# Performance work log

Hardware: AMD Instinct MI355X
Metric: run time of the kernel (lower is better)

## Reference

```python
import jax, jax.numpy as jnp
import numpy as np

D_MODEL = 1024

def setup_inputs() -> dict:
    key = jax.random.key(0)
    ks = jax.random.split(key, 5)
    s = 1.0 / np.sqrt(D_MODEL)  # torch Linear default init scale-ish
    x = jax.random.normal(ks[0], (4, 2048, D_MODEL), dtype=jnp.float32)
    Wq = jax.random.normal(ks[1], (D_MODEL, D_MODEL), dtype=jnp.float32) * s
    Wk = jax.random.normal(ks[2], (D_MODEL, D_MODEL), dtype=jnp.float32) * s
    Wv = jax.random.normal(ks[3], (D_MODEL, D_MODEL), dtype=jnp.float32) * s
    Wo = jax.random.normal(ks[4], (D_MODEL, D_MODEL), dtype=jnp.float32) * s
    z = jnp.zeros((D_MODEL,), dtype=jnp.float32)
    return {"x": x, "Wq": Wq, "bq": z, "Wk": Wk, "bk": z, "Wv": Wv, "bv": z, "Wo": Wo, "bo": z}

def reference(x, Wq, bq, Wk, bk, Wv, bv, Wo, bo):
    # x: (B, S, D). Single-head causal attention, dropout in eval mode (identity).
    B, S, D = x.shape
    Q = jnp.einsum('bsd,ed->bse', x, Wq) + bq
    K = jnp.einsum('bsd,ed->bse', x, Wk) + bk
    V = jnp.einsum('bsd,ed->bse', x, Wv) + bv
    scores = jnp.einsum('bqd,bkd->bqk', Q, K) / jnp.sqrt(jnp.float32(D))
    causal = jnp.tril(jnp.ones((S, S), dtype=bool))  # (S, S)
    scores = jnp.where(causal, scores, -jnp.inf)
    weights = jax.nn.softmax(scores, axis=-1)
    attended = jnp.einsum('bqk,bkd->bqd', weights, V)
    out = jnp.einsum('bsd,ed->bse', attended, Wo) + bo
    return out
```

## Files before the change

kernel.cpp:

```cpp
#include <hip/hip_runtime.h>
#include <cstdint>
#include <cstddef>


#define D_MODEL 1024
#define SEQ     2048
#define BATCH   4

typedef unsigned short u16;
typedef __bf16 bf16_t;
typedef bf16_t bf16x8 __attribute__((ext_vector_type(8)));
typedef float  f32x4  __attribute__((ext_vector_type(4)));
typedef u16    u16x4  __attribute__((ext_vector_type(4)));

__device__ __forceinline__ u16 f2bf(float x) {
  union { float f; uint32_t u; } v; v.f = x;
  uint32_t r = v.u + 0x7fffu + ((v.u >> 16) & 1u);
  return (u16)(r >> 16);
}
__device__ __forceinline__ float bf2f(u16 h) {
  union { uint32_t u; float f; } v; v.u = (uint32_t)h << 16;
  return v.f;
}

__device__ __forceinline__ void gload_lds16(const u16* g, u16* l) {
  __builtin_amdgcn_global_load_lds((__attribute__((address_space(1))) void*)g,
                                   (__attribute__((address_space(3))) void*)l,
                                   16, 0, 0);
}

__device__ __forceinline__ void gemm256(const u16* __restrict__ A,
                                        const u16* __restrict__ B,
                                        int lda, int ldb, int nt,
                                        u16* As, u16* Bs,
                                        f32x4 acc[8][4]) {
  const int tid  = threadIdx.x;
  const int lane = tid & 63, wave = tid >> 6;
  const int frow = lane & 15, kc = lane >> 4;
  const int abase = (wave >> 2) * 128, bbase = (wave & 3) * 64;
  const int r0 = tid >> 2;
  const int k0 = ((tid & 3) ^ ((r0 >> 1) & 3)) * 8;
  const u16* Asrc0 = A + (size_t)r0 * lda + k0;
  const u16* Asrc1 = A + (size_t)(r0 + 128) * lda + k0;
  const u16* Bsrc0 = B + (size_t)r0 * ldb + k0;
  const u16* Bsrc1 = B + (size_t)(r0 + 128) * ldb + k0;
  int aoff[8], boff[4];
#pragma unroll
  for (int i = 0; i < 8; ++i) {
    const int ra = abase + i * 16 + frow;
    aoff[i] = (ra * 4 + (kc ^ ((ra >> 1) & 3))) * 8;
  }
#pragma unroll
  for (int j = 0; j < 4; ++j) {
    const int rb = bbase + j * 16 + frow;
    boff[j] = (rb * 4 + (kc ^ ((rb >> 1) & 3))) * 8;
  }
  auto stage = [&](int t, int bufi) {
    u16* ab = As + bufi * 8192;
    u16* bb = Bs + bufi * 8192;
    const int kb = t * 32;
    gload_lds16(Asrc0 + kb, ab + tid * 8);
    gload_lds16(Asrc1 + kb, ab + 4096 + tid * 8);
    gload_lds16(Bsrc0 + kb, bb + tid * 8);
    gload_lds16(Bsrc1 + kb, bb + 4096 + tid * 8);
  };
  stage(0, 0);
  if (nt > 1) stage(1, 1);
  int cb = 0, sb = 2;
  for (int t = 0; t < nt; ++t) {
    if (t + 1 < nt) asm volatile("s_waitcnt vmcnt(4)" ::: "memory");
    else            asm volatile("s_waitcnt vmcnt(0)" ::: "memory");
    __builtin_amdgcn_s_barrier();
    asm volatile("" ::: "memory");
    if (t + 2 < nt) stage(t + 2, sb);
    const u16* ab = As + cb * 8192;
    const u16* bb = Bs + cb * 8192;
    bf16x8 af[8], bf[4];
#pragma unroll
    for (int j = 0; j < 4; ++j) bf[j] = *(const bf16x8*)(bb + boff[j]);
#pragma unroll
    for (int i = 0; i < 8; ++i) af[i] = *(const bf16x8*)(ab + aoff[i]);
    __builtin_amdgcn_s_setprio(1);
#pragma unroll
    for (int i = 0; i < 8; ++i)
#pragma unroll
      for (int j = 0; j < 4; ++j)
        acc[i][j] = __builtin_amdgcn_mfma_f32_16x16x32_bf16(af[i], bf[j], acc[i][j], 0, 0, 0);
    __builtin_amdgcn_s_setprio(0);
    asm volatile("" ::: "memory");
    cb = (cb == 2) ? 0 : cb + 1;
    sb = (sb == 2) ? 0 : sb + 1;
  }
}

__device__ __forceinline__ void gemm128(const u16* __restrict__ A,
                                        const u16* __restrict__ B,
                                        int lda, int ldb, int nt,
                                        u16* As, u16* Bs,
                                        f32x4 acc[4][2]) {
  const int tid  = threadIdx.x;
  const int lane = tid & 63, wave = tid >> 6;
  const int frow = lane & 15, kc = lane >> 4;
  const int abase = (wave >> 2) * 64, bbase = (wave & 3) * 32;
  const int r0 = tid >> 2;
  const int k0 = ((tid & 3) ^ ((r0 >> 1) & 3)) * 8;
  const u16* Asrc = A + (size_t)r0 * lda + k0;
  const u16* Bsrc = B + (size_t)r0 * ldb + k0;
  int aoff[4], boff[2];
#pragma unroll
  for (int i = 0; i < 4; ++i) {
    const int ra = abase + i * 16 + frow;
    aoff[i] = (ra * 4 + (kc ^ ((ra >> 1) & 3))) * 8;
  }
#pragma unroll
  for (int j = 0; j < 2; ++j) {
    const int rb = bbase + j * 16 + frow;
    boff[j] = (rb * 4 + (kc ^ ((rb >> 1) & 3))) * 8;
  }
  auto stage = [&](int t) {
    u16* ab = As + (t & 3) * 4096;
    u16* bb = Bs + (t & 3) * 4096;
    const int kb = t * 32;
    gload_lds16(Asrc + kb, ab + tid * 8);
    gload_lds16(Bsrc + kb, bb + tid * 8);
  };
  stage(0);
  if (nt > 1) stage(1);
  if (nt > 2) stage(2);
  for (int t = 0; t < nt; ++t) {
    if (t + 2 < nt)      asm volatile("s_waitcnt vmcnt(4)" ::: "memory");
    else if (t + 1 < nt) asm volatile("s_waitcnt vmcnt(2)" ::: "memory");
    else                 asm volatile("s_waitcnt vmcnt(0)" ::: "memory");
    __builtin_amdgcn_s_barrier();
    asm volatile("" ::: "memory");
    if (t + 3 < nt) stage(t + 3);
    const u16* ab = As + (t & 3) * 4096;
    const u16* bb = Bs + (t & 3) * 4096;
    bf16x8 af[4], bf[2];
#pragma unroll
    for (int j = 0; j < 2; ++j) bf[j] = *(const bf16x8*)(bb + boff[j]);
#pragma unroll
    for (int i = 0; i < 4; ++i) af[i] = *(const bf16x8*)(ab + aoff[i]);
    __builtin_amdgcn_s_setprio(1);
#pragma unroll
    for (int i = 0; i < 4; ++i)
#pragma unroll
      for (int j = 0; j < 2; ++j)
        acc[i][j] = __builtin_amdgcn_mfma_f32_16x16x32_bf16(af[i], bf[j], acc[i][j], 0, 0, 0);
    __builtin_amdgcn_s_setprio(0);
    asm volatile("" ::: "memory");
  }
}

__global__ __launch_bounds__(256) void cvt_kernel(const float4* __restrict__ x,
                                                  const float4* __restrict__ wq,
                                                  const float4* __restrict__ wk,
                                                  const float4* __restrict__ wv,
                                                  const float4* __restrict__ wo,
                                                  u16* __restrict__ dst) {
  const int i = blockIdx.x * 256 + threadIdx.x;
  float4 v;
  if (i < 2097152) {
    v = x[i];
  } else {
    const int j = i - 2097152;
    const int w = j >> 18;
    const float4* s = (w == 0) ? wq : (w == 1) ? wk : (w == 2) ? wv : wo;
    v = s[j & 262143];
  }
  u16x4 o = {f2bf(v.x), f2bf(v.y), f2bf(v.z), f2bf(v.w)};
  *(u16x4*)(dst + (size_t)i * 4) = o;
}

__global__ void transposeW_kernel(const u16* __restrict__ src, u16* __restrict__ dst) {
  __shared__ u16 tile[32][33];
  const int r0 = blockIdx.x * 32, c0 = blockIdx.y * 32;
  const int tx = threadIdx.x, ty = threadIdx.y;
#pragma unroll
  for (int r = 0; r < 4; ++r)
    tile[ty + r * 8][tx] = src[(size_t)(r0 + ty + r * 8) * D_MODEL + c0 + tx];
  __syncthreads();
#pragma unroll
  for (int r = 0; r < 4; ++r)
    dst[(size_t)(c0 + ty + r * 8) * D_MODEL + r0 + tx] = tile[tx][ty + r * 8];
}

__global__ __launch_bounds__(512, 2) void stageA_kernel(
    const u16* __restrict__ xb,
    const u16* __restrict__ WqB, const u16* __restrict__ WkB,
    const u16* __restrict__ WoB, const u16* __restrict__ WvT,
    const float* __restrict__ Wo32, const float* __restrict__ bv,
    const float* __restrict__ bq, const float* __restrict__ bk,
    u16* __restrict__ Qb, u16* __restrict__ Kb,
    u16* __restrict__ Wp, float* __restrict__ bp) {
  __shared__ __align__(16) u16 As[24576];
  __shared__ __align__(16) u16 Bs[24576];
  const int blk = blockIdx.x, tid = threadIdx.x;
  const int lane = tid & 63, wave = tid >> 6;
  const int cl = lane & 15, rl = (lane >> 4) * 4;

  if (blk < 256) {
    const int c = blk & 7, i = blk >> 3;
    const int z = i >> 4, w = i & 15;
    const int rt = c * 4 + (w >> 2), ct = w & 3;
    const int row0 = rt * 256, col0 = ct * 256;
    const u16*   W    = z ? WkB : WqB;
    const float* bias = z ? bk : bq;
    u16*         out  = z ? Kb : Qb;
    f32x4 acc[8][4] = {};
    gemm256(xb + (size_t)row0 * D_MODEL, W + (size_t)col0 * D_MODEL,
            D_MODEL, D_MODEL, 32, As, Bs, acc);
    const int abase = (wave >> 2) * 128, bbase = (wave & 3) * 64;
#pragma unroll
    for (int j = 0; j < 4; ++j) {
      const int col = col0 + bbase + j * 16 + cl;
      const float bb = bias[col];
#pragma unroll
      for (int ii = 0; ii < 8; ++ii)
#pragma unroll
        for (int r = 0; r < 4; ++r) {
          const int row = row0 + abase + ii * 16 + rl + r;
          out[(size_t)row * D_MODEL + col] = f2bf(acc[ii][j][r] + bb);
        }
    }
  } else if (blk < 320) {
    const int qq = blk - 256;
    const int t16 = qq >> 2, quad = qq & 3;
    const int f0 = (t16 >> 2) * 256 + (quad >> 1) * 128;
    const int e0 = (t16 & 3) * 256 + (quad & 1) * 128;
    f32x4 acc[4][2] = {};
    gemm128(WoB + (size_t)f0 * D_MODEL, WvT + (size_t)e0 * D_MODEL,
            D_MODEL, D_MODEL, 32, As, Bs, acc);
    const int abase = (wave >> 2) * 64, bbase = (wave & 3) * 32;
#pragma unroll
    for (int j = 0; j < 2; ++j) {
      const int col = e0 + bbase + j * 16 + cl;
#pragma unroll
      for (int ii = 0; ii < 4; ++ii)
#pragma unroll
        for (int r = 0; r < 4; ++r) {
          const int row = f0 + abase + ii * 16 + rl + r;
          Wp[(size_t)row * D_MODEL + col] = f2bf(acc[ii][j][r]);
        }
    }
  } else {
    const int f  = (blk - 320) * 64 + (tid >> 3);
    const int dq = tid & 7;
    const float* row = Wo32 + (size_t)f * D_MODEL + dq * 128;
    const float* bvq = bv + dq * 128;
    float s = 0.f;
#pragma unroll 8
    for (int k = 0; k < 128; ++k) s += row[k] * bvq[k];
    s += __shfl_xor(s, 1);
    s += __shfl_xor(s, 2);
    s += __shfl_xor(s, 4);
    if (dq == 0) bp[f] = s;
  }
}

__global__ __launch_bounds__(512, 2) void stageB_kernel(
    const u16* __restrict__ xb, const u16* __restrict__ Wp,
    const float* __restrict__ bp,
    const u16* __restrict__ Qb, const u16* __restrict__ Kb,
    u16* __restrict__ Vt, u16* __restrict__ Eb, float* __restrict__ rssum) {
  __shared__ __align__(16) u16 As[24576];
  __shared__ __align__(16) u16 Bs[24576];
  const int blk = blockIdx.x, tid = threadIdx.x;
  const int lane = tid & 63, wave = tid >> 6;
  const int cl = lane & 15, rl = (lane >> 4) * 4;

  if (blk < 144) {
    const int c = blk & 7, u = blk >> 3;
    const int b = c >> 1, h = c & 1;
    int qi, ji;
    if (h == 0) {
      if (u < 1)       { qi = 0; ji = u; }
      else if (u < 5)  { qi = 3; ji = u - 1; }
      else if (u < 10) { qi = 4; ji = u - 5; }
      else             { qi = 7; ji = u - 10; }
    } else {
      if (u < 2)       { qi = 1; ji = u; }
      else if (u < 5)  { qi = 2; ji = u - 2; }
      else if (u < 11) { qi = 5; ji = u - 5; }
      else             { qi = 6; ji = u - 11; }
    }
    const u16* A  = Qb + (size_t)(b * SEQ + qi * 256) * D_MODEL;
    const u16* Bt = Kb + (size_t)(b * SEQ + ji * 256) * D_MODEL;
    f32x4 acc[8][4] = {};
    gemm256(A, Bt, D_MODEL, D_MODEL, 32, As, Bs, acc);
    u16* outp = Eb + (size_t)b * SEQ * SEQ;
    float* rs = rssum + b * SEQ;
    const int abase = (wave >> 2) * 128, bbase = (wave & 3) * 64;
#pragma unroll
    for (int ii = 0; ii < 8; ++ii)
#pragma unroll
      for (int r = 0; r < 4; ++r) {
        const int q = qi * 256 + abase + ii * 16 + rl + r;
        float ps = 0.f;
#pragma unroll
        for (int j = 0; j < 4; ++j) {
          const int jj = ji * 256 + bbase + j * 16 + cl;
          u16 h16 = 0;
          if (jj <= q) h16 = f2bf(__expf(acc[ii][j][r] * 0.03125f));
          outp[(size_t)q * SEQ + jj] = h16;
          ps += bf2f(h16);
        }
        ps += __shfl_xor(ps, 1);
        ps += __shfl_xor(ps, 2);
        ps += __shfl_xor(ps, 4);
        ps += __shfl_xor(ps, 8);
        if (cl == 0) atomicAdd(&rs[q], ps);
      }
  } else if (blk < 256) {
    const int v = blk - 144;
    const int rt = v >> 2, ct = v & 3;
    const int row0 = rt * 256, col0 = ct * 256;
    f32x4 acc[8][4] = {};
    gemm256(xb + (size_t)row0 * D_MODEL, Wp + (size_t)col0 * D_MODEL,
            D_MODEL, D_MODEL, 32, As, Bs, acc);
    const int b = row0 >> 11;
    u16* vt = Vt + (size_t)b * D_MODEL * SEQ;
    const int abase = (wave >> 2) * 128, bbase = (wave & 3) * 64;
#pragma unroll
    for (int j = 0; j < 4; ++j) {
      const int col = col0 + bbase + j * 16 + cl;
      const float bb = bp[col];
#pragma unroll
      for (int ii = 0; ii < 8; ++ii) {
        const int s0 = (row0 & 2047) + abase + ii * 16 + rl;
        u16x4 o = {f2bf(acc[ii][j][0] + bb), f2bf(acc[ii][j][1] + bb),
                   f2bf(acc[ii][j][2] + bb), f2bf(acc[ii][j][3] + bb)};
        *(u16x4*)(vt + (size_t)col * SEQ + s0) = o;
      }
    }
  } else {
    const int qq = blk - 256;
    const int t16 = qq >> 2, quad = qq & 3;
    const int rt = 28 + (t16 >> 2), ct = t16 & 3;
    const int row0 = rt * 256 + (quad >> 1) * 128;
    const int col0 = ct * 256 + (quad & 1) * 128;
    f32x4 acc[4][2] = {};
    gemm128(xb + (size_t)row0 * D_MODEL, Wp + (size_t)col0 * D_MODEL,
            D_MODEL, D_MODEL, 32, As, Bs, acc);
    const int b = row0 >> 11;
    u16* vt = Vt + (size_t)b * D_MODEL * SEQ;
    const int abase = (wave >> 2) * 64, bbase = (wave & 3) * 32;
#pragma unroll
    for (int j = 0; j < 2; ++j) {
      const int col = col0 + bbase + j * 16 + cl;
      const float bb = bp[col];
#pragma unroll
      for (int ii = 0; ii < 4; ++ii) {
        const int s0 = (row0 & 2047) + abase + ii * 16 + rl;
        u16x4 o = {f2bf(acc[ii][j][0] + bb), f2bf(acc[ii][j][1] + bb),
                   f2bf(acc[ii][j][2] + bb), f2bf(acc[ii][j][3] + bb)};
        *(u16x4*)(vt + (size_t)col * SEQ + s0) = o;
      }
    }
  }
}

__global__ __launch_bounds__(512, 4) void pv_kernel(const u16* __restrict__ Eb,
                                                    const u16* __restrict__ Vt,
                                                    const float* __restrict__ rssum,
                                                    const float* __restrict__ bo,
                                                    float* __restrict__ Out) {
  __shared__ __align__(16) u16 As[16384];
  __shared__ __align__(16) u16 Bs[16384];
  const int blk = blockIdx.x, tid = threadIdx.x;
  const int rr = blk >> 8, idx = blk & 255;
  const int b = idx >> 6, rest = idx & 63;
  const int dt8 = rest >> 3, m = rest & 7;
  const int qt = rr ? (15 - 2 * m) : (2 * m);
  const u16* A  = Eb + (size_t)b * SEQ * SEQ + (size_t)(qt * 128) * SEQ;
  const u16* Bt = Vt + (size_t)b * D_MODEL * SEQ + (size_t)(dt8 * 128) * SEQ;
  f32x4 acc[4][2] = {};
  gemm128(A, Bt, SEQ, SEQ, (qt + 1) * 4, As, Bs, acc);
  const int lane = tid & 63, wave = tid >> 6;
  const int abase = (wave >> 2) * 64, bbase = (wave & 3) * 32;
  const int cl = lane & 15, rl = (lane >> 4) * 4;
#pragma unroll
  for (int ii = 0; ii < 4; ++ii)
#pragma unroll
    for (int r = 0; r < 4; ++r) {
      const int row = qt * 128 + abase + ii * 16 + rl + r;
      const float invl = 1.0f / rssum[b * SEQ + row];
#pragma unroll
      for (int j = 0; j < 2; ++j) {
        const int col = dt8 * 128 + bbase + j * 16 + cl;
        Out[(size_t)(b * SEQ + row) * D_MODEL + col] = acc[ii][j][r] * invl + bo[col];
      }
    }
}

extern "C" void kernel_launch(void* const* d_in, const int* in_sizes, int n_in,
                              void* d_out, int out_size, void* d_ws, size_t ws_size,
                              hipStream_t stream) {
  const float* x  = (const float*)d_in[0];
  const float* Wq = (const float*)d_in[1];
  const float* bq = (const float*)d_in[2];
  const float* Wk = (const float*)d_in[3];
  const float* bk = (const float*)d_in[4];
  const float* Wv = (const float*)d_in[5];
  const float* bv = (const float*)d_in[6];
  const float* Wo = (const float*)d_in[7];
  const float* bo = (const float*)d_in[8];
  float* out = (float*)d_out;
  char* ws = (char*)d_ws;

  u16*   xb  = (u16*)(ws);
  u16*   Wb  = (u16*)(ws + (16u << 20));
  u16*   Qb  = (u16*)(ws + (24u << 20));
  u16*   Kb  = (u16*)(ws + (40u << 20));
  u16*   Vt  = (u16*)(ws + (56u << 20));
  u16*   Eb  = (u16*)(ws + (72u << 20));
  u16*   WvT = (u16*)(ws + (104u << 20));
  u16*   Wp  = (u16*)(ws + (106u << 20));
  float* bp  = (float*)(ws + (108u << 20));
  float* rssum = (float*)(ws + (20u << 20));

  cvt_kernel<<<12288, 256, 0, stream>>>((const float4*)x, (const float4*)Wq,
                                        (const float4*)Wk, (const float4*)Wv,
                                        (const float4*)Wo, xb);
  transposeW_kernel<<<dim3(32, 32), dim3(32, 8), 0, stream>>>(Wb + (2u << 20), WvT);
  stageA_kernel<<<336, 512, 0, stream>>>(xb, Wb, Wb + (1u << 20), Wb + (3u << 20),
                                         WvT, Wo, bv, bq, bk, Qb, Kb, Wp, bp);
  hipMemsetAsync(rssum, 0, BATCH * SEQ * sizeof(float), stream);
  stageB_kernel<<<320, 512, 0, stream>>>(xb, Wp, bp, Qb, Kb, Vt, Eb, rssum);
  pv_kernel<<<512, 512, 0, stream>>>(Eb, Vt, rssum, bo, out);
}
```

Before: 269.0 us.

## Use BK=64 double-buffered gemm256 and 256x256 tiles in PV kernel

The 256x256 GEMM core now loads K-slices of 64 into two LDS buffers instead of 32-wide slices into a triple buffer. This halves the number of barrier/wait iterations, and the MFMA work is split into interleaved half-steps so LDS reads overlap compute. The PV kernel moves from 128x128 tiles (512 blocks) to 256x256 tiles via gemm256 (128 blocks) for more operand reuse. The cost is larger LDS use, lower PV occupancy, and possible load imbalance, because only 128 causally uneven blocks are launched.

Result: slower. 290.6 us (+8.0%).

```diff
diff --git a/kernel.cpp b/kernel.cpp
--- a/kernel.cpp
+++ b/kernel.cpp
@@ -31,65 +31,94 @@
 
 __device__ __forceinline__ void gemm256(const u16* __restrict__ A,
                                         const u16* __restrict__ B,
-                                        int lda, int ldb, int nt,
+                                        int lda, int ldb, int nt64,
                                         u16* As, u16* Bs,
                                         f32x4 acc[8][4]) {
   const int tid  = threadIdx.x;
   const int lane = tid & 63, wave = tid >> 6;
   const int frow = lane & 15, kc = lane >> 4;
   const int abase = (wave >> 2) * 128, bbase = (wave & 3) * 64;
-  const int r0 = tid >> 2;
-  const int k0 = ((tid & 3) ^ ((r0 >> 1) & 3)) * 8;
-  const u16* Asrc0 = A + (size_t)r0 * lda + k0;
-  const u16* Asrc1 = A + (size_t)(r0 + 128) * lda + k0;
-  const u16* Bsrc0 = B + (size_t)r0 * ldb + k0;
-  const u16* Bsrc1 = B + (size_t)(r0 + 128) * ldb + k0;
+  const int r8 = tid >> 3, cch = tid & 7;
+  const int swz = ((r8 & 1) << 2) | ((r8 >> 1) & 3);
+  const int g8 = (cch ^ swz) * 8;
+  const u16* Arow = A + (size_t)r8 * lda + g8;
+  const u16* Brow = B + (size_t)r8 * ldb + g8;
+  const size_t lda64 = (size_t)64 * lda, ldb64 = (size_t)64 * ldb;
   int aoff[8], boff[4];
 #pragma unroll
   for (int i = 0; i < 8; ++i) {
     const int ra = abase + i * 16 + frow;
-    aoff[i] = (ra * 4 + (kc ^ ((ra >> 1) & 3))) * 8;
+    const int c0 = (kc ^ ((ra >> 1) & 3)) ^ ((ra & 1) << 2);
+    aoff[i] = ra * 64 + c0 * 8;
   }
 #pragma unroll
   for (int j = 0; j < 4; ++j) {
     const int rb = bbase + j * 16 + frow;
-    boff[j] = (rb * 4 + (kc ^ ((rb >> 1) & 3))) * 8;
-  }
-  auto stage = [&](int t, int bufi) {
-    u16* ab = As + bufi * 8192;
-    u16* bb = Bs + bufi * 8192;
-    const int kb = t * 32;
-    gload_lds16(Asrc0 + kb, ab + tid * 8);
-    gload_lds16(Asrc1 + kb, ab + 4096 + tid * 8);
-    gload_lds16(Bsrc0 + kb, bb + tid * 8);
-    gload_lds16(Bsrc1 + kb, bb + 4096 + tid * 8);
+    const int c0 = (kc ^ ((rb >> 1) & 3)) ^ ((rb & 1) << 2);
+    boff[j] = rb * 64 + c0 * 8;
+  }
+  auto stage = [&](int t) {
+    u16* ab = As + (t & 1) * 16384;
+    u16* bb = Bs + (t & 1) * 16384;
+    const int kb = t * 64;
+#pragma unroll
+    for (int L = 0; L < 4; ++L)
+      gload_lds16(Arow + kb + L * lda64, ab + (L * 512 + tid) * 8);
+#pragma unroll
+    for (int L = 0; L < 4; ++L)
+      gload_lds16(Brow + kb + L * ldb64, bb + (L * 512 + tid) * 8);
   };
-  stage(0, 0);
-  if (nt > 1) stage(1, 1);
-  int cb = 0, sb = 2;
-  for (int t = 0; t < nt; ++t) {
-    if (t + 1 < nt) asm volatile("s_waitcnt vmcnt(4)" ::: "memory");
-    else            asm volatile("s_waitcnt vmcnt(0)" ::: "memory");
+  stage(0);
+  for (int t = 0; t < nt64; ++t) {
     __builtin_amdgcn_s_barrier();
-    asm volatile("" ::: "memory");
-    if (t + 2 < nt) stage(t + 2, sb);
-    const u16* ab = As + cb * 8192;
-    const u16* bb = Bs + cb * 8192;
-    bf16x8 af[8], bf[4];
-#pragma unroll
-    for (int j = 0; j < 4; ++j) bf[j] = *(const bf16x8*)(bb + boff[j]);
-#pragma unroll
-    for (int i = 0; i < 8; ++i) af[i] = *(const bf16x8*)(ab + aoff[i]);
+    if (t + 1 < nt64) {
+      stage(t + 1);
+      asm volatile("s_waitcnt vmcnt(8)" ::: "memory");
+    } else {
+      asm volatile("s_waitcnt vmcnt(0)" ::: "memory");
+    }
+    __builtin_amdgcn_s_barrier();
+    const u16* ab = As + (t & 1) * 16384;
+    const u16* bb = Bs + (t & 1) * 16384;
+    bf16x8 a0[4], a1[4], b0[4], b1[4];
+#pragma unroll
+    for (int j = 0; j < 4; ++j) b0[j] = *(const bf16x8*)(bb + boff[j]);
+#pragma unroll
+    for (int i = 0; i < 4; ++i) a0[i] = *(const bf16x8*)(ab + aoff[i]);
+#pragma unroll
+    for (int i = 0; i < 4; ++i) a1[i] = *(const bf16x8*)(ab + aoff[4 + i]);
     __builtin_amdgcn_s_setprio(1);
 #pragma unroll
-    for (int i = 0; i < 8; ++i)
+    for (int i = 0; i < 4; ++i)
 #pragma unroll
       for (int j = 0; j < 4; ++j)
-        acc[i][j] = __builtin_amdgcn_mfma_f32_16x16x32_bf16(af[i], bf[j], acc[i][j], 0, 0, 0);
+        acc[i][j] = __builtin_amdgcn_mfma_f32_16x16x32_bf16(a0[i], b0[j], acc[i][j], 0, 0, 0);
     __builtin_amdgcn_s_setprio(0);
-    asm volatile("" ::: "memory");
-    cb = (cb == 2) ? 0 : cb + 1;
-    sb = (sb == 2) ? 0 : sb + 1;
+#pragma unroll
+    for (int j = 0; j < 4; ++j) b1[j] = *(const bf16x8*)(bb + (boff[j] ^ 32));
+#pragma unroll
+    for (int i = 0; i < 4; ++i) a0[i] = *(const bf16x8*)(ab + (aoff[i] ^ 32));
+    __builtin_amdgcn_s_setprio(1);
+#pragma unroll
+    for (int i = 0; i < 4; ++i)
+#pragma unroll
+      for (int j = 0; j < 4; ++j)
+        acc[4 + i][j] = __builtin_amdgcn_mfma_f32_16x16x32_bf16(a1[i], b0[j], acc[4 + i][j], 0, 0, 0);
+    __builtin_amdgcn_s_setprio(0);
+#pragma unroll
+    for (int i = 0; i < 4; ++i) a1[i] = *(const bf16x8*)(ab + (aoff[4 + i] ^ 32));
+    __builtin_amdgcn_s_setprio(1);
+#pragma unroll
+    for (int i = 0; i < 4; ++i)
+#pragma unroll
+      for (int j = 0; j < 4; ++j)
+        acc[i][j] = __builtin_amdgcn_mfma_f32_16x16x32_bf16(a0[i], b1[j], acc[i][j], 0, 0, 0);
+#pragma unroll
+    for (int i = 0; i < 4; ++i)
+#pragma unroll
+      for (int j = 0; j < 4; ++j)
+        acc[4 + i][j] = __builtin_amdgcn_mfma_f32_16x16x32_bf16(a1[i], b1[j], acc[4 + i][j], 0, 0, 0);
+    __builtin_amdgcn_s_setprio(0);
   }
 }
 
@@ -193,8 +222,8 @@
     const float* __restrict__ bq, const float* __restrict__ bk,
     u16* __restrict__ Qb, u16* __restrict__ Kb,
     u16* __restrict__ Wp, float* __restrict__ bp) {
-  __shared__ __align__(16) u16 As[24576];
-  __shared__ __align__(16) u16 Bs[24576];
+  __shared__ __align__(16) u16 As[32768];
+  __shared__ __align__(16) u16 Bs[32768];
   const int blk = blockIdx.x, tid = threadIdx.x;
   const int lane = tid & 63, wave = tid >> 6;
   const int cl = lane & 15, rl = (lane >> 4) * 4;
@@ -209,7 +238,7 @@
     u16*         out  = z ? Kb : Qb;
     f32x4 acc[8][4] = {};
     gemm256(xb + (size_t)row0 * D_MODEL, W + (size_t)col0 * D_MODEL,
-            D_MODEL, D_MODEL, 32, As, Bs, acc);
+            D_MODEL, D_MODEL, 16, As, Bs, acc);
     const int abase = (wave >> 2) * 128, bbase = (wave & 3) * 64;
 #pragma unroll
     for (int j = 0; j < 4; ++j) {
@@ -263,8 +292,8 @@
     const float* __restrict__ bp,
     const u16* __restrict__ Qb, const u16* __restrict__ Kb,
     u16* __restrict__ Vt, u16* __restrict__ Eb, float* __restrict__ rssum) {
-  __shared__ __align__(16) u16 As[24576];
-  __shared__ __align__(16) u16 Bs[24576];
+  __shared__ __align__(16) u16 As[32768];
+  __shared__ __align__(16) u16 Bs[32768];
   const int blk = blockIdx.x, tid = threadIdx.x;
   const int lane = tid & 63, wave = tid >> 6;
   const int cl = lane & 15, rl = (lane >> 4) * 4;
@@ -287,7 +316,7 @@
     const u16* A  = Qb + (size_t)(b * SEQ + qi * 256) * D_MODEL;
     const u16* Bt = Kb + (size_t)(b * SEQ + ji * 256) * D_MODEL;
     f32x4 acc[8][4] = {};
-    gemm256(A, Bt, D_MODEL, D_MODEL, 32, As, Bs, acc);
+    gemm256(A, Bt, D_MODEL, D_MODEL, 16, As, Bs, acc);
     u16* outp = Eb + (size_t)b * SEQ * SEQ;
     float* rs = rssum + b * SEQ;
     const int abase = (wave >> 2) * 128, bbase = (wave & 3) * 64;
@@ -317,7 +346,7 @@
     const int row0 = rt * 256, col0 = ct * 256;
     f32x4 acc[8][4] = {};
     gemm256(xb + (size_t)row0 * D_MODEL, Wp + (size_t)col0 * D_MODEL,
-            D_MODEL, D_MODEL, 32, As, Bs, acc);
+            D_MODEL, D_MODEL, 16, As, Bs, acc);
     const int b = row0 >> 11;
     u16* vt = Vt + (size_t)b * D_MODEL * SEQ;
     const int abase = (wave >> 2) * 128, bbase = (wave & 3) * 64;
@@ -360,35 +389,35 @@
   }
 }
 
-__global__ __launch_bounds__(512, 4) void pv_kernel(const u16* __restrict__ Eb,
+__global__ __launch_bounds__(512, 2) void pv_kernel(const u16* __restrict__ Eb,
                                                     const u16* __restrict__ Vt,
                                                     const float* __restrict__ rssum,
                                                     const float* __restrict__ bo,
                                                     float* __restrict__ Out) {
-  __shared__ __align__(16) u16 As[16384];
-  __shared__ __align__(16) u16 Bs[16384];
+  __shared__ __align__(16) u16 As[32768];
+  __shared__ __align__(16) u16 Bs[32768];
   const int blk = blockIdx.x, tid = threadIdx.x;
-  const int rr = blk >> 8, idx = blk & 255;
-  const int b = idx >> 6, rest = idx & 63;
-  const int dt8 = rest >> 3, m = rest & 7;
-  const int qt = rr ? (15 - 2 * m) : (2 * m);
-  const u16* A  = Eb + (size_t)b * SEQ * SEQ + (size_t)(qt * 128) * SEQ;
-  const u16* Bt = Vt + (size_t)b * D_MODEL * SEQ + (size_t)(dt8 * 128) * SEQ;
-  f32x4 acc[4][2] = {};
-  gemm128(A, Bt, SEQ, SEQ, (qt + 1) * 4, As, Bs, acc);
+  const int c = blk & 7, i = blk >> 3;
+  const int b  = c >> 1;
+  const int dt = (c & 1) * 2 + (i & 1);
+  const int qt = i >> 1;
+  const u16* A  = Eb + (size_t)b * SEQ * SEQ + (size_t)(qt * 256) * SEQ;
+  const u16* Bt = Vt + (size_t)b * D_MODEL * SEQ + (size_t)(dt * 256) * SEQ;
+  f32x4 acc[8][4] = {};
+  gemm256(A, Bt, SEQ, SEQ, (qt + 1) * 4, As, Bs, acc);
   const int lane = tid & 63, wave = tid >> 6;
-  const int abase = (wave >> 2) * 64, bbase = (wave & 3) * 32;
+  const int abase = (wave >> 2) * 128, bbase = (wave & 3) * 64;
   const int cl = lane & 15, rl = (lane >> 4) * 4;
 #pragma unroll
-  for (int ii = 0; ii < 4; ++ii)
+  for (int ii = 0; ii < 8; ++ii)
 #pragma unroll
     for (int r = 0; r < 4; ++r) {
-      const int row = qt * 128 + abase + ii * 16 + rl + r;
-      const float invl = 1.0f / rssum[b * SEQ + row];
-#pragma unroll
-      for (int j = 0; j < 2; ++j) {
-        const int col = dt8 * 128 + bbase + j * 16 + cl;
-        Out[(size_t)(b * SEQ + row) * D_MODEL + col] = acc[ii][j][r] * invl + bo[col];
+      const int q = qt * 256 + abase + ii * 16 + rl + r;
+      const float invl = 1.0f / rssum[b * SEQ + q];
+#pragma unroll
+      for (int j = 0; j < 4; ++j) {
+        const int col = dt * 256 + bbase + j * 16 + cl;
+        Out[(size_t)(b * SEQ + q) * D_MODEL + col] = acc[ii][j][r] * invl + bo[col];
       }
     }
 }
@@ -427,5 +456,5 @@
                                          WvT, Wo, bv, bq, bk, Qb, Kb, Wp, bp);
   hipMemsetAsync(rssum, 0, BATCH * SEQ * sizeof(float), stream);
   stageB_kernel<<<320, 512, 0, stream>>>(xb, Wp, bp, Qb, Kb, Vt, Eb, rssum);
-  pv_kernel<<<512, 512, 0, stream>>>(Eb, Vt, rssum, bo, out);
-}
+  pv_kernel<<<128, 512, 0, stream>>>(Eb, Vt, rssum, bo, out);
+}
```
